# Performance work log

Measured on AMD Instinct MI355X. Metric: run time of the kernel, lower is better.

## Reference

```python
import jax, jax.numpy as jnp
import numpy as np

NUM_GRAPHS = 512

def _add_self_loops(edge_index, n):
    loop = jnp.arange(n, dtype=edge_index.dtype)
    row = jnp.concatenate([edge_index[0], loop])
    col = jnp.concatenate([edge_index[1], loop])
    return row, col

def _gcn_conv(x, W, b, row, col, norm, n):
    h = x @ W                              # [N, H] dense transform
    msgs = h[row] * norm[:, None]          # gather + normalize, [E+N, H]
    out = jax.ops.segment_sum(msgs, col, num_segments=n)
    return out + b

def setup_inputs() -> dict:
    key = jax.random.key(0)
    ks = jax.random.split(key, 10)
    N, E, F_IN, H, C = 50000, 800000, 128, 128, 16
    s = 1.0 / np.sqrt(H)
    return {
        "x": jax.random.normal(ks[0], (N, F_IN), dtype=jnp.float32),
        "edge_index": jax.random.randint(ks[1], (2, E), 0, N, dtype=jnp.int64),
        "batch": jnp.sort(jax.random.randint(ks[2], (N,), 0, NUM_GRAPHS, dtype=jnp.int64)),
        "W1": jax.random.normal(ks[3], (F_IN, H), dtype=jnp.float32) * s,
        "b1": jnp.zeros((H,), dtype=jnp.float32),
        "W2": jax.random.normal(ks[4], (H, H), dtype=jnp.float32) * s,
        "b2": jnp.zeros((H,), dtype=jnp.float32),
        "W3": jax.random.normal(ks[5], (H, H), dtype=jnp.float32) * s,
        "b3": jnp.zeros((H,), dtype=jnp.float32),
        "lin_W": jax.random.normal(ks[6], (H, C), dtype=jnp.float32) * s,
        "lin_b": jnp.zeros((C,), dtype=jnp.float32),
    }

def reference(x, edge_index, batch, W1, b1, W2, b2, W3, b3, lin_W, lin_b):
    n = x.shape[0]
    row, col = _add_self_loops(edge_index, n)
    # symmetric degree normalization (computed once, shared by all layers)
    deg = jax.ops.segment_sum(jnp.ones_like(col, dtype=x.dtype), col, num_segments=n)
    dinv = jnp.where(deg > 0, jax.lax.rsqrt(deg), 0.0)
    norm = dinv[row] * dinv[col]           # [E+N]

    h = jax.nn.relu(_gcn_conv(x, W1, b1, row, col, norm, n))
    h = jax.nn.relu(_gcn_conv(h, W2, b2, row, col, norm, n))
    h = _gcn_conv(h, W3, b3, row, col, norm, n)

    # global mean pool over graphs in the batch
    pooled = jax.ops.segment_sum(h, batch, num_segments=NUM_GRAPHS)
    cnt = jax.ops.segment_sum(jnp.ones((n,), dtype=h.dtype), batch, num_segments=NUM_GRAPHS)
    pooled = pooled / jnp.maximum(cnt, 1.0)[:, None]

    # dropout is identity in eval mode
    return pooled @ lin_W + lin_b          # [NUM_GRAPHS, C]
```

## Files before the change

kernel.cpp:

```cpp
#include <hip/hip_runtime.h>
#include <hip/hip_bf16.h>

#define FEAT 128
#define NGRAPH 512
#define NCLS 16


__device__ inline unsigned short f2bf(float f) {
    __hip_bfloat16 h = __float2bfloat16(f);
    return *(unsigned short*)&h;
}
__device__ inline unsigned int pk2(float a, float b) {
    return (unsigned int)f2bf(a) | ((unsigned int)f2bf(b) << 16);
}
__device__ inline void unpk2(unsigned int u, float& lo, float& hi) {
    lo = __uint_as_float(u << 16);
    hi = __uint_as_float(u & 0xffff0000u);
}


__global__ void k_hist(const int* __restrict__ col, int* __restrict__ hist, int E) {
    int i = blockIdx.x * blockDim.x + threadIdx.x;
    if (i < E) atomicAdd(&hist[col[i]], 1);
}

__global__ void k_dinv(const int* __restrict__ hist, float* __restrict__ dinv, int N) {
    int i = blockIdx.x * blockDim.x + threadIdx.x;
    if (i < N) dinv[i] = rsqrtf((float)(hist[i] + 1));
}

__global__ void k_scanA(const int* __restrict__ hist, int* __restrict__ partial, int N) {
    __shared__ int s[256];
    int i = blockIdx.x * 256 + threadIdx.x;
    s[threadIdx.x] = (i < N) ? hist[i] : 0;
    __syncthreads();
    for (int off = 128; off > 0; off >>= 1) {
        if (threadIdx.x < off) s[threadIdx.x] += s[threadIdx.x + off];
        __syncthreads();
    }
    if (threadIdx.x == 0) partial[blockIdx.x] = s[0];
}

__global__ void k_scanB(int* __restrict__ partial, int nb) {
    __shared__ int s[256];
    int t = threadIdx.x;
    int orig = (t < nb) ? partial[t] : 0;
    s[t] = orig;
    __syncthreads();
    for (int off = 1; off < 256; off <<= 1) {
        int v = (t >= off) ? s[t - off] : 0;
        __syncthreads();
        s[t] += v;
        __syncthreads();
    }
    if (t < nb) partial[t] = s[t] - orig;
}

__global__ void k_scanC(const int* __restrict__ hist, const int* __restrict__ partial,
                        int* __restrict__ start, int* __restrict__ cur, int N) {
    __shared__ int s[256];
    int t = threadIdx.x;
    int i = blockIdx.x * 256 + t;
    int orig = (i < N) ? hist[i] : 0;
    s[t] = orig;
    __syncthreads();
    for (int off = 1; off < 256; off <<= 1) {
        int v = (t >= off) ? s[t - off] : 0;
        __syncthreads();
        s[t] += v;
        __syncthreads();
    }
    if (i < N) {
        int ex = s[t] - orig + partial[blockIdx.x];
        start[i] = ex;
        cur[i] = ex;
    }
}

__global__ void k_fill(const int* __restrict__ row, const int* __restrict__ col,
                       const float* __restrict__ dinv, int* __restrict__ cur,
                       int* __restrict__ csr_row, float* __restrict__ csr_w, int E) {
    int i = blockIdx.x * blockDim.x + threadIdx.x;
    if (i >= E) return;
    int r = row[i], c = col[i];
    int pos = atomicAdd(&cur[c], 1);
    csr_row[pos] = r;
    csr_w[pos] = dinv[r] * dinv[c];
}


#define BM 64
#define BK 32

__global__ __launch_bounds__(256) void k_gemm(const float* __restrict__ A,
                                              const float* __restrict__ W,
                                              unsigned int* __restrict__ Cbf, int M) {
    __shared__ float As[BM][BK + 1];
    __shared__ float Ws[BK][FEAT + 4];
    int tid = threadIdx.x;
    int m0 = blockIdx.x * BM;
    int ty = tid >> 4, tx = tid & 15;
    float acc[4][8] = {};

    for (int kt = 0; kt < FEAT; kt += BK) {
        for (int u = tid; u < BM * BK / 4; u += 256) {
            int ar = u >> 3, ac = (u & 7) * 4;
            int gr = m0 + ar;
            float4 v = make_float4(0.f, 0.f, 0.f, 0.f);
            if (gr < M) v = *(const float4*)&A[(size_t)gr * FEAT + kt + ac];
            As[ar][ac + 0] = v.x; As[ar][ac + 1] = v.y;
            As[ar][ac + 2] = v.z; As[ar][ac + 3] = v.w;
        }
        for (int u = tid; u < BK * FEAT / 4; u += 256) {
            int wr = u >> 5, wc = (u & 31) * 4;
            float4 v = *(const float4*)&W[(size_t)(kt + wr) * FEAT + wc];
            Ws[wr][wc + 0] = v.x; Ws[wr][wc + 1] = v.y;
            Ws[wr][wc + 2] = v.z; Ws[wr][wc + 3] = v.w;
        }
        __syncthreads();
        #pragma unroll
        for (int kk = 0; kk < BK; ++kk) {
            float a0 = As[ty * 4 + 0][kk];
            float a1 = As[ty * 4 + 1][kk];
            float a2 = As[ty * 4 + 2][kk];
            float a3 = As[ty * 4 + 3][kk];
            float b[8];
            *(float4*)&b[0] = *(float4*)&Ws[kk][tx * 8];
            *(float4*)&b[4] = *(float4*)&Ws[kk][tx * 8 + 4];
            #pragma unroll
            for (int j = 0; j < 8; ++j) {
                acc[0][j] = fmaf(a0, b[j], acc[0][j]);
                acc[1][j] = fmaf(a1, b[j], acc[1][j]);
                acc[2][j] = fmaf(a2, b[j], acc[2][j]);
                acc[3][j] = fmaf(a3, b[j], acc[3][j]);
            }
        }
        __syncthreads();
    }
    #pragma unroll
    for (int i = 0; i < 4; ++i) {
        int gr = m0 + ty * 4 + i;
        if (gr < M) {
            uint4 o;
            o.x = pk2(acc[i][0], acc[i][1]);
            o.y = pk2(acc[i][2], acc[i][3]);
            o.z = pk2(acc[i][4], acc[i][5]);
            o.w = pk2(acc[i][6], acc[i][7]);
            *(uint4*)&Cbf[(size_t)gr * (FEAT / 2) + tx * 4] = o;
        }
    }
}


__global__ __launch_bounds__(256) void k_agg(const uint2* __restrict__ tbf,
                                             const int* __restrict__ csr_row,
                                             const float* __restrict__ csr_w,
                                             const int* __restrict__ start,
                                             const int* __restrict__ endp,
                                             const float* __restrict__ dinv,
                                             const float* __restrict__ bias,
                                             float* __restrict__ h, int N, int do_relu) {
    int t = threadIdx.x;
    int v = blockIdx.x * 8 + (t >> 5);
    if (v >= N) return;
    int lane = t & 31;

    float a0, a1, a2, a3;
    {
        float dv = dinv[v];
        float ws = dv * dv;
        uint2 sv = tbf[(size_t)v * 32 + lane];
        float f0, f1, f2, f3;
        unpk2(sv.x, f0, f1); unpk2(sv.y, f2, f3);
        a0 = f0 * ws; a1 = f1 * ws; a2 = f2 * ws; a3 = f3 * ws;
    }

    int s = start[v], e = endp[v];
    int p = s;
    for (; p + 4 <= e; p += 4) {
        int r0 = csr_row[p], r1 = csr_row[p + 1], r2 = csr_row[p + 2], r3 = csr_row[p + 3];
        float w0 = csr_w[p], w1 = csr_w[p + 1], w2 = csr_w[p + 2], w3 = csr_w[p + 3];
        uint2 g0 = tbf[(size_t)r0 * 32 + lane];
        uint2 g1 = tbf[(size_t)r1 * 32 + lane];
        uint2 g2 = tbf[(size_t)r2 * 32 + lane];
        uint2 g3 = tbf[(size_t)r3 * 32 + lane];
        float f0, f1, f2, f3;
        unpk2(g0.x, f0, f1); unpk2(g0.y, f2, f3);
        a0 = fmaf(f0, w0, a0); a1 = fmaf(f1, w0, a1); a2 = fmaf(f2, w0, a2); a3 = fmaf(f3, w0, a3);
        unpk2(g1.x, f0, f1); unpk2(g1.y, f2, f3);
        a0 = fmaf(f0, w1, a0); a1 = fmaf(f1, w1, a1); a2 = fmaf(f2, w1, a2); a3 = fmaf(f3, w1, a3);
        unpk2(g2.x, f0, f1); unpk2(g2.y, f2, f3);
        a0 = fmaf(f0, w2, a0); a1 = fmaf(f1, w2, a1); a2 = fmaf(f2, w2, a2); a3 = fmaf(f3, w2, a3);
        unpk2(g3.x, f0, f1); unpk2(g3.y, f2, f3);
        a0 = fmaf(f0, w3, a0); a1 = fmaf(f1, w3, a1); a2 = fmaf(f2, w3, a2); a3 = fmaf(f3, w3, a3);
    }
    for (; p < e; ++p) {
        int r = csr_row[p];
        float w = csr_w[p];
        uint2 g = tbf[(size_t)r * 32 + lane];
        float f0, f1, f2, f3;
        unpk2(g.x, f0, f1); unpk2(g.y, f2, f3);
        a0 = fmaf(f0, w, a0); a1 = fmaf(f1, w, a1); a2 = fmaf(f2, w, a2); a3 = fmaf(f3, w, a3);
    }

    float4 b4 = *(const float4*)&bias[lane * 4];
    a0 += b4.x; a1 += b4.y; a2 += b4.z; a3 += b4.w;
    if (do_relu) {
        a0 = fmaxf(a0, 0.f); a1 = fmaxf(a1, 0.f);
        a2 = fmaxf(a2, 0.f); a3 = fmaxf(a3, 0.f);
    }
    *(float4*)&h[(size_t)v * FEAT + lane * 4] = make_float4(a0, a1, a2, a3);
}


__global__ void k_gcnt(const int* __restrict__ batch, int* __restrict__ gcnt, int N) {
    int v = blockIdx.x * blockDim.x + threadIdx.x;
    if (v < N) atomicAdd(&gcnt[batch[v]], 1);
}

__global__ void k_goff(const int* __restrict__ gcnt, int* __restrict__ goff,
                       float* __restrict__ cntf) {
    __shared__ int s[NGRAPH];
    int t = threadIdx.x;
    int v = gcnt[t];
    s[t] = v;
    __syncthreads();
    for (int off = 1; off < NGRAPH; off <<= 1) {
        int u = (t >= off) ? s[t - off] : 0;
        __syncthreads();
        s[t] += u;
        __syncthreads();
    }
    goff[t] = s[t] - v;
    cntf[t] = (float)v;
}

__global__ __launch_bounds__(128) void k_pool(const float* __restrict__ h,
                                              const int* __restrict__ goff,
                                              const int* __restrict__ gcnt,
                                              float* __restrict__ pooled) {
    int g = blockIdx.x, t = threadIdx.x;
    int s = goff[g], n = gcnt[g];
    float acc = 0.f;
    for (int i = 0; i < n; ++i) acc += h[(size_t)(s + i) * FEAT + t];
    pooled[g * FEAT + t] = acc / fmaxf((float)n, 1.f);
}

__global__ void k_final(const float* __restrict__ pooled,
                        const float* __restrict__ linW, const float* __restrict__ linb,
                        float* __restrict__ out) {
    int idx = blockIdx.x * blockDim.x + threadIdx.x;
    if (idx >= NGRAPH * NCLS) return;
    int g = idx >> 4, c = idx & 15;
    float acc = 0.f;
    #pragma unroll 8
    for (int jj = 0; jj < FEAT; ++jj)
        acc = fmaf(pooled[g * FEAT + jj], linW[jj * NCLS + c], acc);
    out[idx] = acc + linb[c];
}


extern "C" void kernel_launch(void* const* d_in, const int* in_sizes, int n_in,
                              void* d_out, int out_size, void* d_ws, size_t ws_size,
                              hipStream_t stream) {
    const float* x    = (const float*)d_in[0];
    const int*   ei   = (const int*)d_in[1];
    const int*   batch= (const int*)d_in[2];
    const float* W1   = (const float*)d_in[3];
    const float* b1   = (const float*)d_in[4];
    const float* W2   = (const float*)d_in[5];
    const float* b2   = (const float*)d_in[6];
    const float* W3   = (const float*)d_in[7];
    const float* b3   = (const float*)d_in[8];
    const float* linW = (const float*)d_in[9];
    const float* linb = (const float*)d_in[10];
    float* out = (float*)d_out;

    const int N = in_sizes[0] / FEAT;
    const int E = in_sizes[1] / 2;
    const int* row = ei;
    const int* col = ei + E;

    char* p = (char*)d_ws;
    auto alloc = [&](size_t bytes) { void* r = (void*)p; p += (bytes + 255) & ~(size_t)255; return r; };
    int*   hist    = (int*)  alloc((size_t)N * 4);
    int*   start   = (int*)  alloc((size_t)N * 4);
    int*   cur     = (int*)  alloc((size_t)N * 4);
    float* dinv    = (float*)alloc((size_t)N * 4);
    int*   csr_row = (int*)  alloc((size_t)E * 4);
    float* csr_w   = (float*)alloc((size_t)E * 4);
    int*   partial = (int*)  alloc(4096);
    unsigned int* tbf = (unsigned int*)alloc((size_t)N * FEAT * 2);
    float* h       = (float*)alloc((size_t)N * FEAT * 4);
    float* pooled  = (float*)alloc((size_t)NGRAPH * FEAT * 4);
    float* cntf    = (float*)alloc((size_t)NGRAPH * 4);
    int*   gcnt    = (int*)  alloc((size_t)NGRAPH * 4);
    int*   goff    = (int*)  alloc((size_t)NGRAPH * 4);

    hipMemsetAsync(hist, 0, (size_t)N * 4, stream);
    hipMemsetAsync(gcnt, 0, (size_t)NGRAPH * 4, stream);

    const int nscan = (N + 255) / 256;

    k_hist <<<(E + 255) / 256, 256, 0, stream>>>(col, hist, E);
    k_dinv <<<nscan, 256, 0, stream>>>(hist, dinv, N);
    k_scanA<<<nscan, 256, 0, stream>>>(hist, partial, N);
    k_scanB<<<1, 256, 0, stream>>>(partial, nscan);
    k_scanC<<<nscan, 256, 0, stream>>>(hist, partial, start, cur, N);
    k_fill <<<(E + 255) / 256, 256, 0, stream>>>(row, col, dinv, cur, csr_row, csr_w, E);
    k_gcnt <<<nscan, 256, 0, stream>>>(batch, gcnt, N);
    k_goff <<<1, NGRAPH, 0, stream>>>(gcnt, goff, cntf);

    const int gblk = (N + BM - 1) / BM;
    const int ablk = (N + 7) / 8;

    k_gemm<<<gblk, 256, 0, stream>>>(x, W1, tbf, N);
    k_agg <<<ablk, 256, 0, stream>>>((const uint2*)tbf, csr_row, csr_w, start, cur, dinv, b1, h, N, 1);
    k_gemm<<<gblk, 256, 0, stream>>>(h, W2, tbf, N);
    k_agg <<<ablk, 256, 0, stream>>>((const uint2*)tbf, csr_row, csr_w, start, cur, dinv, b2, h, N, 1);
    k_gemm<<<gblk, 256, 0, stream>>>(h, W3, tbf, N);
    k_agg <<<ablk, 256, 0, stream>>>((const uint2*)tbf, csr_row, csr_w, start, cur, dinv, b3, h, N, 0);

    k_pool <<<NGRAPH, 128, 0, stream>>>(h, goff, gcnt, pooled);
    k_final<<<(NGRAPH * NCLS + 255) / 256, 256, 0, stream>>>(pooled, linW, linb, out);
}
```

Baseline: 477.3 us.

## Use split-bf16 MFMA GEMM and fold degree normalization into GEMM epilogue

Replaces the FP32 SIMT shared-memory GEMM with MFMA 16x16x32 bf16 instructions. A 3-term hi/lo bf16 split keeps near-FP32 accuracy, and weights are pre-split into the MFMA fragment layout by a new kernel. The symmetric normalization is refactored so the GEMM scales each output row by dinv[row] and aggregation scales the sum by dinv[v]. This removes the per-edge weight array and its loads in aggregation. The GEMM epilogue now writes scattered 2-byte stores, which may be less efficient than the previous vectorized stores.

```diff
diff --git a/kernel.cpp b/kernel.cpp
--- a/kernel.cpp
+++ b/kernel.cpp
@@ -5,13 +5,16 @@
 #define NGRAPH 512
 #define NCLS 16
 
+typedef __attribute__((ext_vector_type(8))) short bf16x8;
+typedef __attribute__((ext_vector_type(4))) float f32x4;
+
 
 __device__ inline unsigned short f2bf(float f) {
     __hip_bfloat16 h = __float2bfloat16(f);
     return *(unsigned short*)&h;
 }
-__device__ inline unsigned int pk2(float a, float b) {
-    return (unsigned int)f2bf(a) | ((unsigned int)f2bf(b) << 16);
+__device__ inline float bf2f(unsigned short u) {
+    return __uint_as_float((unsigned int)u << 16);
 }
 __device__ inline void unpk2(unsigned int u, float& lo, float& hi) {
     lo = __uint_as_float(u << 16);
@@ -78,75 +81,85 @@
 }
 
 __global__ void k_fill(const int* __restrict__ row, const int* __restrict__ col,
-                       const float* __restrict__ dinv, int* __restrict__ cur,
-                       int* __restrict__ csr_row, float* __restrict__ csr_w, int E) {
+                       int* __restrict__ cur, int* __restrict__ csr_row, int E) {
     int i = blockIdx.x * blockDim.x + threadIdx.x;
     if (i >= E) return;
     int r = row[i], c = col[i];
     int pos = atomicAdd(&cur[c], 1);
     csr_row[pos] = r;
-    csr_w[pos] = dinv[r] * dinv[c];
-}
-
-
-#define BM 64
-#define BK 32
+}
+
+
+__global__ void k_wsplit(const float* __restrict__ W1, const float* __restrict__ W2,
+                         const float* __restrict__ W3,
+                         bf16x8* __restrict__ whi, bf16x8* __restrict__ wlo) {
+    int tid = blockIdx.x * 256 + threadIdx.x;
+    int layer = tid >> 11;
+    int r = tid & 2047;
+    int kt = r >> 9, cb = (r >> 6) & 7, lane = r & 63;
+    const float* W = (layer == 0) ? W1 : (layer == 1) ? W2 : W3;
+    bf16x8 hi, lo;
+    #pragma unroll
+    for (int j = 0; j < 8; ++j) {
+        float w = W[(size_t)(kt * 32 + (lane >> 4) * 8 + j) * FEAT + cb * 16 + (lane & 15)];
+        unsigned short hb = f2bf(w);
+        hi[j] = (short)hb;
+        lo[j] = (short)f2bf(w - bf2f(hb));
+    }
+    size_t idx = (size_t)layer * 2048 + (kt * 8 + cb) * 64 + lane;
+    whi[idx] = hi;
+    wlo[idx] = lo;
+}
+
 
 __global__ __launch_bounds__(256) void k_gemm(const float* __restrict__ A,
-                                              const float* __restrict__ W,
-                                              unsigned int* __restrict__ Cbf, int M) {
-    __shared__ float As[BM][BK + 1];
-    __shared__ float Ws[BK][FEAT + 4];
+                                              const bf16x8* __restrict__ Whi,
+                                              const bf16x8* __restrict__ Wlo,
+                                              const float* __restrict__ dinv,
+                                              unsigned short* __restrict__ tbf, int M) {
     int tid = threadIdx.x;
-    int m0 = blockIdx.x * BM;
-    int ty = tid >> 4, tx = tid & 15;
-    float acc[4][8] = {};
-
-    for (int kt = 0; kt < FEAT; kt += BK) {
-        for (int u = tid; u < BM * BK / 4; u += 256) {
-            int ar = u >> 3, ac = (u & 7) * 4;
-            int gr = m0 + ar;
-            float4 v = make_float4(0.f, 0.f, 0.f, 0.f);
-            if (gr < M) v = *(const float4*)&A[(size_t)gr * FEAT + kt + ac];
-            As[ar][ac + 0] = v.x; As[ar][ac + 1] = v.y;
-            As[ar][ac + 2] = v.z; As[ar][ac + 3] = v.w;
+    int wave = tid >> 6, lane = tid & 63;
+    int m0 = blockIdx.x * 64 + wave * 16;
+    int aclamp = min(m0 + (lane & 15), M - 1);
+    int kgrp = lane >> 4;
+
+    f32x4 acc[8];
+    #pragma unroll
+    for (int c = 0; c < 8; ++c) acc[c] = (f32x4){0.f, 0.f, 0.f, 0.f};
+
+    #pragma unroll
+    for (int kt = 0; kt < 4; ++kt) {
+        const float* ap = A + (size_t)aclamp * FEAT + kt * 32 + kgrp * 8;
+        float av[8];
+        *(float4*)&av[0] = *(const float4*)ap;
+        *(float4*)&av[4] = *(const float4*)(ap + 4);
+        bf16x8 ahi, alo;
+        #pragma unroll
+        for (int j = 0; j < 8; ++j) {
+            unsigned short hb = f2bf(av[j]);
+            ahi[j] = (short)hb;
+            alo[j] = (short)f2bf(av[j] - bf2f(hb));
         }
-        for (int u = tid; u < BK * FEAT / 4; u += 256) {
-            int wr = u >> 5, wc = (u & 31) * 4;
-            float4 v = *(const float4*)&W[(size_t)(kt + wr) * FEAT + wc];
-            Ws[wr][wc + 0] = v.x; Ws[wr][wc + 1] = v.y;
-            Ws[wr][wc + 2] = v.z; Ws[wr][wc + 3] = v.w;
+        #pragma unroll
+        for (int cb = 0; cb < 8; ++cb) {
+            bf16x8 bh = Whi[(kt * 8 + cb) * 64 + lane];
+            bf16x8 bl = Wlo[(kt * 8 + cb) * 64 + lane];
+            acc[cb] = __builtin_amdgcn_mfma_f32_16x16x32_bf16(ahi, bh, acc[cb], 0, 0, 0);
+            acc[cb] = __builtin_amdgcn_mfma_f32_16x16x32_bf16(alo, bh, acc[cb], 0, 0, 0);
+            acc[cb] = __builtin_amdgcn_mfma_f32_16x16x32_bf16(ahi, bl, acc[cb], 0, 0, 0);
         }
-        __syncthreads();
-        #pragma unroll
-        for (int kk = 0; kk < BK; ++kk) {
-            float a0 = As[ty * 4 + 0][kk];
-            float a1 = As[ty * 4 + 1][kk];
-            float a2 = As[ty * 4 + 2][kk];
-            float a3 = As[ty * 4 + 3][kk];
-            float b[8];
-            *(float4*)&b[0] = *(float4*)&Ws[kk][tx * 8];
-            *(float4*)&b[4] = *(float4*)&Ws[kk][tx * 8 + 4];
+    }
+
+    int rbase = m0 + (lane >> 4) * 4;
+    int colb = lane & 15;
+    #pragma unroll
+    for (int r = 0; r < 4; ++r) {
+        int gr = rbase + r;
+        if (gr < M) {
+            float dv = dinv[gr];
             #pragma unroll
-            for (int j = 0; j < 8; ++j) {
-                acc[0][j] = fmaf(a0, b[j], acc[0][j]);
-                acc[1][j] = fmaf(a1, b[j], acc[1][j]);
-                acc[2][j] = fmaf(a2, b[j], acc[2][j]);
-                acc[3][j] = fmaf(a3, b[j], acc[3][j]);
-            }
-        }
-        __syncthreads();
-    }
-    #pragma unroll
-    for (int i = 0; i < 4; ++i) {
-        int gr = m0 + ty * 4 + i;
-        if (gr < M) {
-            uint4 o;
-            o.x = pk2(acc[i][0], acc[i][1]);
-            o.y = pk2(acc[i][2], acc[i][3]);
-            o.z = pk2(acc[i][4], acc[i][5]);
-            o.w = pk2(acc[i][6], acc[i][7]);
-            *(uint4*)&Cbf[(size_t)gr * (FEAT / 2) + tx * 4] = o;
+            for (int cb = 0; cb < 8; ++cb)
+                tbf[(size_t)gr * FEAT + cb * 16 + colb] = f2bf(acc[cb][r] * dv);
         }
     }
 }
@@ -154,7 +167,6 @@
 
 __global__ __launch_bounds__(256) void k_agg(const uint2* __restrict__ tbf,
                                              const int* __restrict__ csr_row,
-                                             const float* __restrict__ csr_w,
                                              const int* __restrict__ start,
                                              const int* __restrict__ endp,
                                              const float* __restrict__ dinv,
@@ -167,44 +179,40 @@
 
     float a0, a1, a2, a3;
     {
-        float dv = dinv[v];
-        float ws = dv * dv;
         uint2 sv = tbf[(size_t)v * 32 + lane];
-        float f0, f1, f2, f3;
-        unpk2(sv.x, f0, f1); unpk2(sv.y, f2, f3);
-        a0 = f0 * ws; a1 = f1 * ws; a2 = f2 * ws; a3 = f3 * ws;
+        unpk2(sv.x, a0, a1); unpk2(sv.y, a2, a3);
     }
 
     int s = start[v], e = endp[v];
     int p = s;
     for (; p + 4 <= e; p += 4) {
         int r0 = csr_row[p], r1 = csr_row[p + 1], r2 = csr_row[p + 2], r3 = csr_row[p + 3];
-        float w0 = csr_w[p], w1 = csr_w[p + 1], w2 = csr_w[p + 2], w3 = csr_w[p + 3];
         uint2 g0 = tbf[(size_t)r0 * 32 + lane];
         uint2 g1 = tbf[(size_t)r1 * 32 + lane];
         uint2 g2 = tbf[(size_t)r2 * 32 + lane];
         uint2 g3 = tbf[(size_t)r3 * 32 + lane];
         float f0, f1, f2, f3;
         unpk2(g0.x, f0, f1); unpk2(g0.y, f2, f3);
-        a0 = fmaf(f0, w0, a0); a1 = fmaf(f1, w0, a1); a2 = fmaf(f2, w0, a2); a3 = fmaf(f3, w0, a3);
+        a0 += f0; a1 += f1; a2 += f2; a3 += f3;
         unpk2(g1.x, f0, f1); unpk2(g1.y, f2, f3);
-        a0 = fmaf(f0, w1, a0); a1 = fmaf(f1, w1, a1); a2 = fmaf(f2, w1, a2); a3 = fmaf(f3, w1, a3);
+        a0 += f0; a1 += f1; a2 += f2; a3 += f3;
         unpk2(g2.x, f0, f1); unpk2(g2.y, f2, f3);
-        a0 = fmaf(f0, w2, a0); a1 = fmaf(f1, w2, a1); a2 = fmaf(f2, w2, a2); a3 = fmaf(f3, w2, a3);
+        a0 += f0; a1 += f1; a2 += f2; a3 += f3;
         unpk2(g3.x, f0, f1); unpk2(g3.y, f2, f3);
-        a0 = fmaf(f0, w3, a0); a1 = fmaf(f1, w3, a1); a2 = fmaf(f2, w3, a2); a3 = fmaf(f3, w3, a3);
+        a0 += f0; a1 += f1; a2 += f2; a3 += f3;
     }
     for (; p < e; ++p) {
         int r = csr_row[p];
-        float w = csr_w[p];
         uint2 g = tbf[(size_t)r * 32 + lane];
         float f0, f1, f2, f3;
         unpk2(g.x, f0, f1); unpk2(g.y, f2, f3);
-        a0 = fmaf(f0, w, a0); a1 = fmaf(f1, w, a1); a2 = fmaf(f2, w, a2); a3 = fmaf(f3, w, a3);
-    }
-
+        a0 += f0; a1 += f1; a2 += f2; a3 += f3;
+    }
+
+    float dv = dinv[v];
     float4 b4 = *(const float4*)&bias[lane * 4];
-    a0 += b4.x; a1 += b4.y; a2 += b4.z; a3 += b4.w;
+    a0 = fmaf(a0, dv, b4.x); a1 = fmaf(a1, dv, b4.y);
+    a2 = fmaf(a2, dv, b4.z); a3 = fmaf(a3, dv, b4.w);
     if (do_relu) {
         a0 = fmaxf(a0, 0.f); a1 = fmaxf(a1, 0.f);
         a2 = fmaxf(a2, 0.f); a3 = fmaxf(a3, 0.f);
@@ -288,10 +296,11 @@
     int*   cur     = (int*)  alloc((size_t)N * 4);
     float* dinv    = (float*)alloc((size_t)N * 4);
     int*   csr_row = (int*)  alloc((size_t)E * 4);
-    float* csr_w   = (float*)alloc((size_t)E * 4);
     int*   partial = (int*)  alloc(4096);
-    unsigned int* tbf = (unsigned int*)alloc((size_t)N * FEAT * 2);
+    unsigned short* tbf = (unsigned short*)alloc((size_t)N * FEAT * 2);
     float* h       = (float*)alloc((size_t)N * FEAT * 4);
+    bf16x8* whi    = (bf16x8*)alloc(3 * 2048 * sizeof(bf16x8));
+    bf16x8* wlo    = (bf16x8*)alloc(3 * 2048 * sizeof(bf16x8));
     float* pooled  = (float*)alloc((size_t)NGRAPH * FEAT * 4);
     float* cntf    = (float*)alloc((size_t)NGRAPH * 4);
     int*   gcnt    = (int*)  alloc((size_t)NGRAPH * 4);
@@ -302,24 +311,25 @@
 
     const int nscan = (N + 255) / 256;
 
-    k_hist <<<(E + 255) / 256, 256, 0, stream>>>(col, hist, E);
-    k_dinv <<<nscan, 256, 0, stream>>>(hist, dinv, N);
-    k_scanA<<<nscan, 256, 0, stream>>>(hist, partial, N);
-    k_scanB<<<1, 256, 0, stream>>>(partial, nscan);
-    k_scanC<<<nscan, 256, 0, stream>>>(hist, partial, start, cur, N);
-    k_fill <<<(E + 255) / 256, 256, 0, stream>>>(row, col, dinv, cur, csr_row, csr_w, E);
-    k_gcnt <<<nscan, 256, 0, stream>>>(batch, gcnt, N);
-    k_goff <<<1, NGRAPH, 0, stream>>>(gcnt, goff, cntf);
-
-    const int gblk = (N + BM - 1) / BM;
+    k_hist  <<<(E + 255) / 256, 256, 0, stream>>>(col, hist, E);
+    k_dinv  <<<nscan, 256, 0, stream>>>(hist, dinv, N);
+    k_scanA <<<nscan, 256, 0, stream>>>(hist, partial, N);
+    k_scanB <<<1, 256, 0, stream>>>(partial, nscan);
+    k_scanC <<<nscan, 256, 0, stream>>>(hist, partial, start, cur, N);
+    k_fill  <<<(E + 255) / 256, 256, 0, stream>>>(row, col, cur, csr_row, E);
+    k_wsplit<<<24, 256, 0, stream>>>(W1, W2, W3, whi, wlo);
+    k_gcnt  <<<nscan, 256, 0, stream>>>(batch, gcnt, N);
+    k_goff  <<<1, NGRAPH, 0, stream>>>(gcnt, goff, cntf);
+
+    const int gblk = (N + 63) / 64;
     const int ablk = (N + 7) / 8;
 
-    k_gemm<<<gblk, 256, 0, stream>>>(x, W1, tbf, N);
-    k_agg <<<ablk, 256, 0, stream>>>((const uint2*)tbf, csr_row, csr_w, start, cur, dinv, b1, h, N, 1);
-    k_gemm<<<gblk, 256, 0, stream>>>(h, W2, tbf, N);
-    k_agg <<<ablk, 256, 0, stream>>>((const uint2*)tbf, csr_row, csr_w, start, cur, dinv, b2, h, N, 1);
-    k_gemm<<<gblk, 256, 0, stream>>>(h, W3, tbf, N);
-    k_agg <<<ablk, 256, 0, stream>>>((const uint2*)tbf, csr_row, csr_w, start, cur, dinv, b3, h, N, 0);
+    k_gemm<<<gblk, 256, 0, stream>>>(x, whi,        wlo,        dinv, tbf, N);
+    k_agg <<<ablk, 256, 0, stream>>>((const uint2*)tbf, csr_row, start, cur, dinv, b1, h, N, 1);
+    k_gemm<<<gblk, 256, 0, stream>>>(h, whi + 2048, wlo + 2048, dinv, tbf, N);
+    k_agg <<<ablk, 256, 0, stream>>>((const uint2*)tbf, csr_row, start, cur, dinv, b2, h, N, 1);
+    k_gemm<<<gblk, 256, 0, stream>>>(h, whi + 4096, wlo + 4096, dinv, tbf, N);
+    k_agg <<<ablk, 256, 0, stream>>>((const uint2*)tbf, csr_row, start, cur, dinv, b3, h, N, 0);
 
     k_pool <<<NGRAPH, 128, 0, stream>>>(h, goff, gcnt, pooled);
     k_final<<<(NGRAPH * NCLS + 255) / 256, 256, 0, stream>>>(pooled, linW, linb, out);
```

After: 426.0 us. 10.7% less time.
